# Kernel tuning notes

Measured on AMD Instinct MI355X. Metric: run time of the kernel, lower is better.

The kernel has to match this reference:

```python
import jax, jax.numpy as jnp
import numpy as np

B, L = 2, 2048
DIM, VOCAB, NL = 1024, 32000, 4
DSTATE, DCONV, EXPAND, HEADDIM = 128, 4, 2, 64
DIN = EXPAND * DIM            # 2048
H = DIN // HEADDIM            # 32 heads
CONVDIM = DIN + 2 * DSTATE    # 2304
DPROJ = 2 * DIN + 2 * DSTATE + H  # 4384
FFN = 4 * DIM                 # 4096
Q = 128                       # SSD chunk size
EPS = 1e-6


def _rms(x):
    return x * jax.lax.rsqrt(jnp.mean(x * x, axis=-1, keepdims=True) + EPS)


def _causal_conv(x, w, b):
    # x [B,L,C], depthwise causal conv, w [C,DCONV], b [C]
    y = jax.lax.conv_general_dilated(
        x.transpose(0, 2, 1), w[:, None, :], (1,), [(DCONV - 1, 0)],
        dimension_numbers=('NCH', 'OIH', 'NCH'), feature_group_count=CONVDIM)
    return (y + b[:, None]).transpose(0, 2, 1)


def _ssd(x, dt, A, Bm, Cm):
    # Exact selective scan h_t = h_{t-1}*exp(dt_t*A) + dt_t * x_t B_t ; y_t = C_t . h_t
    # computed in chunked (SSD) matmul form. x [b,l,h,p], dt [b,l,h], A [h], Bm/Cm [b,l,n]
    b, l, h, p = x.shape
    n = Bm.shape[-1]
    c = l // Q
    xr = x.reshape(b, c, Q, h, p)
    dtr = dt.reshape(b, c, Q, h)
    ar = (dt * A).reshape(b, c, Q, h)          # per-step log-decay (<= 0)
    Br = Bm.reshape(b, c, Q, n)
    Cr = Cm.reshape(b, c, Q, n)
    ca = jnp.cumsum(ar, axis=2)                # inclusive cumulative log-decay
    # ---- intra-chunk: causal decay-weighted 'attention' ----
    cah = ca.transpose(0, 1, 3, 2)             # [b,c,h,Q]
    idx = jnp.arange(Q)
    mask = idx[:, None] >= idx[None, :]
    diff = jnp.where(mask[None, None, None], cah[..., :, None] - cah[..., None, :], -jnp.inf)
    M = jnp.exp(diff)                          # [b,c,h,Q,Q]
    CB = jnp.einsum('bcin,bcjn->bcij', Cr, Br)
    T = CB[:, :, None] * M                     # [b,c,h,Q,Q]
    y_intra = jnp.einsum('bchij,bcjh,bcjhp->bcihp', T, dtr, xr)
    # ---- chunk-final states ----
    w = jnp.exp(ca[:, :, -1:, :] - ca) * dtr   # [b,c,Q,h]
    states = jnp.einsum('bcjh,bcjn,bcjhp->bchpn', w, Br, xr)
    chunk_decay = jnp.exp(ca[:, :, -1, :])     # [b,c,h]
    def step(s, inp):
        cd, st = inp
        prev = s
        s = s * cd[:, :, None, None] + st
        return s, prev
    s0 = jnp.zeros((b, h, p, n), x.dtype)
    _, s_prev = jax.lax.scan(step, s0, (chunk_decay.transpose(1, 0, 2),
                                        states.transpose(1, 0, 2, 3, 4)))
    s_prev = s_prev.transpose(1, 0, 2, 3, 4)   # [b,c,h,p,n] state entering each chunk
    y_inter = jnp.einsum('bcih,bcin,bchpn->bcihp', jnp.exp(ca), Cr, s_prev)
    return (y_intra + y_inter).reshape(b, l, h, p)


def _mamba(x, Wi, cw, cb, dtb, Alog, Dp, nw, Wo):
    bsz, sl, _ = x.shape
    zxbcdt = x @ Wi.T                          # [b,l,DPROJ]
    z = zxbcdt[..., :DIN]
    xBC = zxbcdt[..., DIN:DIN + CONVDIM]
    dtraw = zxbcdt[..., DIN + CONVDIM:]
    xBC = jax.nn.silu(_causal_conv(xBC, cw, cb))
    xs = xBC[..., :DIN]
    Bm = xBC[..., DIN:DIN + DSTATE]
    Cm = xBC[..., DIN + DSTATE:]
    dt = jax.nn.softplus(dtraw + dtb)
    A = -jnp.exp(Alog)
    x4 = xs.reshape(bsz, sl, H, HEADDIM)
    y = _ssd(x4, dt, A, Bm, Cm) + Dp[None, None, :, None] * x4
    y = y.reshape(bsz, sl, DIN)
    yg = y * jax.nn.silu(z)                    # gated RMSNorm (norm_before_gate=False)
    y = _rms(yg) * nw
    return y @ Wo.T


def _forward(tokens, embedding, lm_head_bias, in_proj_w, conv_w, conv_b,
             dt_bias, A_log, D, mnorm_w, out_proj_w, u_w, v_w, o_w):
    x = embedding[tokens]
    for li in range(NL):
        for _ in range(2):  # original applies each (mamba, ffn) pair twice
            x = _rms(x)
            x = x + _mamba(x, in_proj_w[li], conv_w[li], conv_b[li], dt_bias[li],
                           A_log[li], D[li], mnorm_w[li], out_proj_w[li])
            x = _rms(x)
            x = x + ((x @ u_w[li].T) * (x @ v_w[li].T)) @ o_w[li].T  # SGLU, dropout=0
    return x @ embedding.T + lm_head_bias      # tied lm_head


def setup_inputs():
    key = jax.random.key(0)
    ks = jax.random.split(key, 16)
    s = 0.02
    return {
        'tokens': jax.random.randint(ks[0], (B, L), 0, VOCAB),
        'embedding': jax.random.normal(ks[1], (VOCAB, DIM), jnp.float32) * s,
        'lm_head_bias': jnp.zeros((VOCAB,), jnp.float32),
        'in_proj_w': jax.random.normal(ks[2], (NL, DPROJ, DIM), jnp.float32) * s,
        'conv_w': jax.random.normal(ks[3], (NL, CONVDIM, DCONV), jnp.float32) * 0.2,
        'conv_b': jnp.zeros((NL, CONVDIM), jnp.float32),
        'dt_bias': jax.random.normal(ks[4], (NL, H), jnp.float32) * 0.3 - 3.0,
        'A_log': jnp.log(jax.random.uniform(ks[5], (NL, H), jnp.float32, 1.0, 16.0)),
        'D': jnp.ones((NL, H), jnp.float32) + 0.1 * jax.random.normal(ks[6], (NL, H), jnp.float32),
        'mnorm_w': jnp.ones((NL, DIN), jnp.float32),
        'out_proj_w': jax.random.normal(ks[7], (NL, DIM, DIN), jnp.float32) * s,
        'u_w': jax.random.normal(ks[8], (NL, FFN, DIM), jnp.float32) * s,
        'v_w': jax.random.normal(ks[9], (NL, FFN, DIM), jnp.float32) * s,
        'o_w': jax.random.normal(ks[10], (NL, DIM, FFN), jnp.float32) * s,
    }


def reference(tokens, embedding, lm_head_bias, in_proj_w, conv_w, conv_b,
              dt_bias, A_log, D, mnorm_w, out_proj_w, u_w, v_w, o_w):
    return _forward(tokens, embedding, lm_head_bias, in_proj_w, conv_w, conv_b,
                    dt_bias, A_log, D, mnorm_w, out_proj_w, u_w, v_w, o_w)
```

## Files before the change

### kernel.cpp

```cpp
#include <hip/hip_runtime.h>
#include <hip/hip_bf16.h>

#define BSZ 2
#define LSEQ 2048
#define DIM 1024
#define VOCAB 32000
#define NLAYER 4
#define DSTATE 128
#define DCONV 4
#define HEADDIM 64
#define DIN 2048
#define NH 32
#define CONVDIM 2304
#define DPROJ 4384
#define FFN 4096
#define QLEN 128
#define NTOK 4096
#define NCHUNK 32
#define CPB 16
#define DTOFF 4352

#define SMEM_BYTES 147456
#define SMEM2 131072

using f32x4 = __attribute__((ext_vector_type(4))) float;
using f16   = _Float16;
using f16x4 = __attribute__((ext_vector_type(4))) _Float16;
using f16x8 = __attribute__((ext_vector_type(8))) _Float16;

__device__ __forceinline__ void gld16(const void* g, void* l) {
  __builtin_amdgcn_global_load_lds(
      (const __attribute__((address_space(1))) unsigned int*)g,
      (__attribute__((address_space(3))) unsigned int*)l, 16, 0, 0);
}

__device__ __forceinline__ void swz_tiles(int& bx, int& by) {
  const int nx = gridDim.x, ny = gridDim.y;
  const int nwg = nx * ny;
  int bid = blockIdx.y * nx + blockIdx.x;
  if ((nwg & 7) == 0) bid = (bid & 7) * (nwg >> 3) + (bid >> 3);
  const int CW = 8;
  const int nchx = nx / CW;
  const int per = CW * ny;
  const int ch = bid / per;
  if (ch < nchx) {
    int wi = bid - ch * per;
    bx = ch * CW + (wi & (CW - 1));
    by = wi / CW;
  } else {
    int tb = bid - nchx * per;
    int tw = nx - nchx * CW;
    bx = nchx * CW + (tb % tw);
    by = tb / tw;
  }
}

template <int MODE>
__global__ __launch_bounds__(512, 2) void gemm_p(
    const f16* __restrict__ A, const f16* __restrict__ B,
    f16* __restrict__ Cg, float* __restrict__ Cf,
    float* __restrict__ dtr, const float* __restrict__ bias,
    int N, int Ksub, int lda, int ldb, int ldc)
{
  extern __shared__ char smem[];
  const int tid  = threadIdx.x;
  const int lane = tid & 63;
  const int wid  = tid >> 6;
  int bx, by; swz_tiles(bx, by);
  const int m0 = by * 256;
  const int n0 = bx * 128;
  const size_t kbase = (size_t)blockIdx.z * Ksub;
  if (gridDim.z > 1) Cg += (size_t)blockIdx.z * (size_t)gridDim.y * 256 * ldc;
  const int NT = Ksub >> 6;

  int arA[4], acA[4];
#pragma unroll
  for (int L = 0; L < 4; ++L) {
    int q = L * 512 + tid;
    int row = q >> 3;
    arA[L] = m0 + row;
    acA[L] = ((q & 7) ^ (row & 7)) << 3;
  }
  int brB[2], bcB[2];
#pragma unroll
  for (int L = 0; L < 2; ++L) {
    int q = L * 512 + tid;
    int row = q >> 3;
    int r = n0 + row; if (r > N - 1) r = N - 1;
    brB[L] = r;
    bcB[L] = ((q & 7) ^ (row & 7)) << 3;
  }

  auto stage = [&](int tt) {
    const int b = tt - (tt / 3) * 3;
    char* Ad = smem + b * 32768;
    char* Bd = smem + 98304 + b * 16384;
    const int kb = tt << 6;
#pragma unroll
    for (int L = 0; L < 4; ++L)
      gld16(A + (size_t)arA[L] * lda + kbase + kb + acA[L], Ad + (L * 512 + tid) * 16);
#pragma unroll
    for (int L = 0; L < 2; ++L)
      gld16(B + (size_t)brB[L] * ldb + kbase + kb + bcB[L], Bd + (L * 512 + tid) * 16);
  };

  const int wm = (wid >> 1) << 6;
  const int wn = (wid & 1) << 6;
  const int fr = lane & 15;
  const int kg = lane >> 4;

  f32x4 acc[4][4] = {};

  stage(0);
  stage(1);

  for (int t = 0; t < NT; ++t) {
    const int b = t - (t / 3) * 3;
    if (t + 1 < NT) {
      asm volatile("s_waitcnt vmcnt(6)" ::: "memory");
    } else {
      asm volatile("s_waitcnt vmcnt(0)" ::: "memory");
    }
    __builtin_amdgcn_s_barrier();
    asm volatile("" ::: "memory");
    if (t + 2 < NT) stage(t + 2);
    const f16* Ab = (const f16*)(smem + b * 32768);
    const f16* Bb = (const f16*)(smem + 98304 + b * 16384);
#pragma unroll
    for (int s = 0; s < 2; ++s) {
      f16x8 af[4], bf[4];
#pragma unroll
      for (int j = 0; j < 4; ++j) {
        int row = wm + j * 16 + fr;
        int g = kg + s * 4;
        af[j] = *(const f16x8*)&Ab[row * 64 + ((g ^ (row & 7)) << 3)];
      }
#pragma unroll
      for (int i = 0; i < 4; ++i) {
        int row = wn + i * 16 + fr;
        int g = kg + s * 4;
        bf[i] = *(const f16x8*)&Bb[row * 64 + ((g ^ (row & 7)) << 3)];
      }
      __builtin_amdgcn_s_setprio(1);
#pragma unroll
      for (int i = 0; i < 4; ++i)
#pragma unroll
        for (int j = 0; j < 4; ++j)
          acc[i][j] = __builtin_amdgcn_mfma_f32_16x16x32_f16(bf[i], af[j], acc[i][j], 0, 0, 0);
      __builtin_amdgcn_s_setprio(0);
    }
    asm volatile("" ::: "memory");
  }

  const int c4 = kg << 2;
#pragma unroll
  for (int i = 0; i < 4; ++i) {
    const int col = n0 + wn + i * 16 + c4;
    if (col >= N) continue;
#pragma unroll
    for (int j = 0; j < 4; ++j) {
      const int row = m0 + wm + j * 16 + fr;
      if constexpr (MODE == 1) {
        f32x4 bv = bias ? *(const f32x4*)(bias + col) : f32x4{0, 0, 0, 0};
        *(f32x4*)(Cf + (size_t)row * ldc + col) = acc[i][j] + bv;
      } else {
        f16x4 h;
#pragma unroll
        for (int r = 0; r < 4; ++r) h[r] = (f16)acc[i][j][r];
        *(f16x4*)(Cg + (size_t)row * ldc + col) = h;
        if (dtr && col >= DTOFF)
          *(f32x4*)(dtr + (size_t)row * NH + (col - DTOFF)) = acc[i][j];
      }
    }
  }
}

__global__ __launch_bounds__(512, 2) void gemm_uv2(
    const f16* __restrict__ A, const f16* __restrict__ Bu, const f16* __restrict__ Bv,
    f16* __restrict__ Gh)
{
  extern __shared__ char smem[];
  const int tid  = threadIdx.x;
  const int lane = tid & 63;
  const int wid  = tid >> 6;
  int bx, by; swz_tiles(bx, by);
  const int m0 = by * 256;
  const int n0 = bx * 128;
  const int NT = DIM >> 6;

  int arA[4], acA[4];
  const f16* bp[4];
  int bcB[4];
#pragma unroll
  for (int L = 0; L < 4; ++L) {
    int q = L * 512 + tid;
    int row = q >> 3;
    arA[L] = m0 + row;
    acA[L] = ((q & 7) ^ (row & 7)) << 3;
    bcB[L] = acA[L];
    bp[L] = (row < 128) ? (Bu + (size_t)(n0 + row) * DIM)
                        : (Bv + (size_t)(n0 + row - 128) * DIM);
  }

  auto stage = [&](int tt) {
    const int b = tt & 1;
    char* Ad = smem + b * 65536;
    char* Bd = Ad + 32768;
    const int kb = tt << 6;
#pragma unroll
    for (int L = 0; L < 4; ++L)
      gld16(A + (size_t)arA[L] * DIM + kb + acA[L], Ad + (L * 512 + tid) * 16);
#pragma unroll
    for (int L = 0; L < 4; ++L)
      gld16(bp[L] + kb + bcB[L], Bd + (L * 512 + tid) * 16);
  };

  const int wm = (wid >> 1) << 6;
  const int wn = (wid & 1) << 6;
  const int fr = lane & 15;
  const int kg = lane >> 4;

  f32x4 accu[4][4] = {}, accv[4][4] = {};

  stage(0);

  for (int t = 0; t < NT; ++t) {
    if (t + 1 < NT) {
      stage(t + 1);
      asm volatile("s_waitcnt vmcnt(8)" ::: "memory");
    } else {
      asm volatile("s_waitcnt vmcnt(0)" ::: "memory");
    }
    __builtin_amdgcn_s_barrier();
    asm volatile("" ::: "memory");
    const f16* Ab = (const f16*)(smem + (t & 1) * 65536);
    const f16* Bb = Ab + 16384;
#pragma unroll
    for (int s = 0; s < 2; ++s) {
      const int g = kg + s * 4;
      f16x8 af[4], bfu[4], bfv[4];
#pragma unroll
      for (int j = 0; j < 4; ++j) {
        int row = wm + j * 16 + fr;
        af[j] = *(const f16x8*)&Ab[row * 64 + ((g ^ (row & 7)) << 3)];
      }
#pragma unroll
      for (int i = 0; i < 4; ++i) {
        int ru = wn + i * 16 + fr;
        int rv = 128 + wn + i * 16 + fr;
        bfu[i] = *(const f16x8*)&Bb[ru * 64 + ((g ^ (ru & 7)) << 3)];
        bfv[i] = *(const f16x8*)&Bb[rv * 64 + ((g ^ (rv & 7)) << 3)];
      }
      __builtin_amdgcn_s_setprio(1);
#pragma unroll
      for (int i = 0; i < 4; ++i)
#pragma unroll
        for (int j = 0; j < 4; ++j) {
          accu[i][j] = __builtin_amdgcn_mfma_f32_16x16x32_f16(bfu[i], af[j], accu[i][j], 0, 0, 0);
          accv[i][j] = __builtin_amdgcn_mfma_f32_16x16x32_f16(bfv[i], af[j], accv[i][j], 0, 0, 0);
        }
      __builtin_amdgcn_s_setprio(0);
    }
    asm volatile("" ::: "memory");
    __builtin_amdgcn_s_barrier();
    asm volatile("" ::: "memory");
  }

  const int c4 = kg << 2;
#pragma unroll
  for (int i = 0; i < 4; ++i) {
    const int col = n0 + wn + i * 16 + c4;
#pragma unroll
    for (int j = 0; j < 4; ++j) {
      const int row = m0 + wm + j * 16 + fr;
      f16x4 h;
#pragma unroll
      for (int r = 0; r < 4; ++r)
        h[r] = (f16)(accu[i][j][r] * accv[i][j][r]);
      *(f16x4*)(Gh + (size_t)row * FFN + col) = h;
    }
  }
}

template <bool DORMS>
__global__ __launch_bounds__(256) void reduce_rms(const f16* __restrict__ parts,
                                                  const float* __restrict__ resid,
                                                  float* __restrict__ xn,
                                                  f16* __restrict__ outh, int np)
{
  const int row = blockIdx.x, tid = threadIdx.x;
  const size_t base = (size_t)row * DIM + tid * 4;
  f32x4 s = *(const f32x4*)(resid + base);
  for (int p = 0; p < np; ++p) {
    f16x4 pv = *(const f16x4*)(parts + (size_t)p * (NTOK * DIM) + base);
#pragma unroll
    for (int c = 0; c < 4; ++c) s[c] += (float)pv[c];
  }
  if constexpr (!DORMS) {
    f16x4 h;
#pragma unroll
    for (int c = 0; c < 4; ++c) h[c] = (f16)s[c];
    *(f16x4*)(outh + base) = h;
    return;
  }
  float ss = s[0] * s[0] + s[1] * s[1] + s[2] * s[2] + s[3] * s[3];
  for (int o = 32; o; o >>= 1) ss += __shfl_down(ss, o);
  __shared__ float red[4];
  if ((tid & 63) == 0) red[tid >> 6] = ss;
  __syncthreads();
  ss = red[0] + red[1] + red[2] + red[3];
  const float sc = rsqrtf(ss * (1.f / 1024.f) + 1e-6f);
  f32x4 o4 = s * sc;
  *(f32x4*)(xn + base) = o4;
  f16x4 h;
#pragma unroll
  for (int c = 0; c < 4; ++c) h[c] = (f16)o4[c];
  *(f16x4*)(outh + base) = h;
}

__global__ __launch_bounds__(256) void cvt_f2h_k(const float* __restrict__ src,
                                                 f16* __restrict__ dst, int n)
{
  for (size_t i = ((size_t)blockIdx.x * 256 + threadIdx.x) * 4; i < (size_t)n;
       i += (size_t)gridDim.x * 1024) {
    f32x4 v = *(const f32x4*)(src + i);
    f16x4 o;
#pragma unroll
    for (int c = 0; c < 4; ++c) o[c] = (f16)v[c];
    *(f16x4*)(dst + i) = o;
  }
}

__global__ __launch_bounds__(256) void cvt_wts(
    const float* __restrict__ inw, const float* __restrict__ outw,
    const float* __restrict__ uw, const float* __restrict__ vw,
    const float* __restrict__ ow,
    f16* __restrict__ w_in, f16* __restrict__ w_out,
    f16* __restrict__ w_uv, f16* __restrict__ w_o)
{
  const int b = blockIdx.x;
  const float* src; f16* dst;
  if (b < 17536) {
    int li = b / 4384, ib = b - li * 4384;
    src = inw  + (size_t)li * 4489216 + (size_t)ib * 1024;
    dst = w_in + (size_t)li * 4489216 + (size_t)ib * 1024;
  } else if (b < 25728) {
    int lb = b - 17536, li = lb >> 11, ib = lb & 2047;
    src = outw  + (size_t)li * 2097152 + (size_t)ib * 1024;
    dst = w_out + (size_t)li * 2097152 + (size_t)ib * 1024;
  } else if (b < 42112) {
    int lb = b - 25728, li = lb >> 12, ib = lb & 4095;
    src = uw   + (size_t)li * 4194304 + (size_t)ib * 1024;
    dst = w_uv + (size_t)li * 8388608 + (size_t)ib * 1024;
  } else if (b < 58496) {
    int lb = b - 42112, li = lb >> 12, ib = lb & 4095;
    src = vw   + (size_t)li * 4194304 + (size_t)ib * 1024;
    dst = w_uv + (size_t)li * 8388608 + 4194304 + (size_t)ib * 1024;
  } else {
    int lb = b - 58496, li = lb >> 12, ib = lb & 4095;
    src = ow  + (size_t)li * 4194304 + (size_t)ib * 1024;
    dst = w_o + (size_t)li * 4194304 + (size_t)ib * 1024;
  }
  const size_t i = (size_t)threadIdx.x * 4;
  f32x4 v = *(const f32x4*)(src + i);
  f16x4 o;
#pragma unroll
  for (int c = 0; c < 4; ++c) o[c] = (f16)v[c];
  *(f16x4*)(dst + i) = o;
}

__global__ __launch_bounds__(256) void gather_k(const int* __restrict__ tok,
                                                const float* __restrict__ emb,
                                                float* __restrict__ x)
{
  const int row = blockIdx.x;
  const int t = tok[row];
  const f32x4* s = (const f32x4*)(emb + (size_t)t * DIM);
  f32x4* d = (f32x4*)(x + (size_t)row * DIM);
  d[threadIdx.x] = s[threadIdx.x];
}

__global__ __launch_bounds__(256) void rms1024(const float* __restrict__ in,
                                               float* __restrict__ outf,
                                               f16* __restrict__ outh)
{
  const int row = blockIdx.x, tid = threadIdx.x;
  f32x4 v = ((const f32x4*)(in + (size_t)row * DIM))[tid];
  float ss = v[0] * v[0] + v[1] * v[1] + v[2] * v[2] + v[3] * v[3];
  for (int o = 32; o; o >>= 1) ss += __shfl_down(ss, o);
  __shared__ float red[4];
  if ((tid & 63) == 0) red[tid >> 6] = ss;
  __syncthreads();
  ss = red[0] + red[1] + red[2] + red[3];
  const float sc = rsqrtf(ss * (1.f / 1024.f) + 1e-6f);
  f32x4 o4 = v * sc;
  ((f32x4*)(outf + (size_t)row * DIM))[tid] = o4;
  f16x4 h;
#pragma unroll
  for (int c = 0; c < 4; ++c) h[c] = (f16)o4[c];
  ((f16x4*)(outh + (size_t)row * DIM))[tid] = h;
}

__global__ __launch_bounds__(256) void convdt(const f16* __restrict__ zx,
                                              const float* __restrict__ dtrw,
                                              const float* __restrict__ cw,
                                              const float* __restrict__ cbias,
                                              const float* __restrict__ dtb,
                                              const float* __restrict__ alog,
                                              f16* __restrict__ xbc,
                                              float* __restrict__ dt,
                                              float* __restrict__ ca)
{
  if (blockIdx.x < 576) {
    const int sid = blockIdx.x * 256 + threadIdx.x;
    const int c0 = (sid % 576) * 4;
    const int t0 = (sid / 576) * 16;
    float w[4][4], bs[4];
#pragma unroll
    for (int cc = 0; cc < 4; ++cc) {
      f32x4 wv = *(const f32x4*)(cw + (size_t)(c0 + cc) * 4);
      w[cc][0] = wv[0]; w[cc][1] = wv[1]; w[cc][2] = wv[2]; w[cc][3] = wv[3];
      bs[cc] = cbias[c0 + cc];
    }
    const int l0 = t0 & (LSEQ - 1);
    float x3[4] = {}, x2[4] = {}, x1[4] = {};
    if (l0 != 0) {
      f16x4 a = *(const f16x4*)(zx + (size_t)(t0 - 3) * DPROJ + DIN + c0);
      f16x4 b = *(const f16x4*)(zx + (size_t)(t0 - 2) * DPROJ + DIN + c0);
      f16x4 d = *(const f16x4*)(zx + (size_t)(t0 - 1) * DPROJ + DIN + c0);
#pragma unroll
      for (int c = 0; c < 4; ++c) { x3[c] = (float)a[c]; x2[c] = (float)b[c]; x1[c] = (float)d[c]; }
    }
    for (int i = 0; i < 16; ++i) {
      const int t = t0 + i;
      f16x4 xcv = *(const f16x4*)(zx + (size_t)t * DPROJ + DIN + c0);
      f16x4 o;
#pragma unroll
      for (int cc = 0; cc < 4; ++cc) {
        float xc = (float)xcv[cc];
        float a = bs[cc] + x3[cc] * w[cc][0] + x2[cc] * w[cc][1] +
                  x1[cc] * w[cc][2] + xc * w[cc][3];
        o[cc] = (f16)(a / (1.f + expf(-a)));
        x3[cc] = x2[cc]; x2[cc] = x1[cc]; x1[cc] = xc;
      }
      *(f16x4*)(xbc + (size_t)t * CONVDIM + c0) = o;
    }
  } else {
    const int loc = (threadIdx.x >> 7) * 128;
    const int u = (blockIdx.x - 576) * 2 + (threadIdx.x >> 7);
    const int bc = u >> 5, h = u & 31, q = threadIdx.x & 127;
    const int t = bc * 128 + q;
    float raw = dtrw[(size_t)t * NH + h] + dtb[h];
    float d = raw > 20.f ? raw : log1pf(expf(raw));
    dt[t * 32 + h] = d;
    float a = -expf(alog[h]) * d;
    __shared__ float s[256];
    s[loc + q] = a;
    __syncthreads();
    for (int off = 1; off < 128; off <<= 1) {
      float v = (q >= off) ? s[loc + q - off] : 0.f;
      __syncthreads();
      s[loc + q] += v;
      __syncthreads();
    }
    ca[(size_t)u * 128 + q] = s[loc + q];
  }
}

__global__ __launch_bounds__(256) void cb_mfma(const f16* __restrict__ xbc,
                                               float* __restrict__ CBo)
{
  const int bc = blockIdx.x;
  __shared__ f16 Cm[128 * 72], Bm[128 * 72];
  const int tid = threadIdx.x, lane = tid & 63, wid = tid >> 6;
  const int fr = lane & 15, kg = lane >> 4;
  f32x4 acc[2][8] = {};
  const int i = tid & 127;
  const f16* rowp = xbc + (size_t)(bc * 128 + i) * CONVDIM + DIN;

  for (int kh = 0; kh < 2; ++kh) {
#pragma unroll
    for (int it = 0; it < 8; ++it) {
      int idx = it * 256 + tid;
      int n0 = (idx >> 7) * 4;
      *(f16x4*)&Bm[i * 72 + n0] = *(const f16x4*)(rowp + kh * 64 + n0);
      *(f16x4*)&Cm[i * 72 + n0] = *(const f16x4*)(rowp + DSTATE + kh * 64 + n0);
    }
    __syncthreads();
#pragma unroll
    for (int kf = 0; kf < 2; ++kf) {
      const int ko = kf * 32 + kg * 8;
      f16x8 cf[2], bf[8];
#pragma unroll
      for (int ii = 0; ii < 2; ++ii)
        cf[ii] = *(const f16x8*)&Cm[((wid * 2 + ii) * 16 + fr) * 72 + ko];
#pragma unroll
      for (int jj = 0; jj < 8; ++jj)
        bf[jj] = *(const f16x8*)&Bm[(jj * 16 + fr) * 72 + ko];
      __builtin_amdgcn_s_setprio(1);
#pragma unroll
      for (int ii = 0; ii < 2; ++ii)
#pragma unroll
        for (int jj = 0; jj < 8; ++jj)
          acc[ii][jj] = __builtin_amdgcn_mfma_f32_16x16x32_f16(cf[ii], bf[jj], acc[ii][jj], 0, 0, 0);
      __builtin_amdgcn_s_setprio(0);
    }
    __syncthreads();
  }
  float* out = CBo + (size_t)bc * 16384;
#pragma unroll
  for (int ii = 0; ii < 2; ++ii) {
    const int i0 = (wid * 2 + ii) * 16 + kg * 4;
#pragma unroll
    for (int jj = 0; jj < 8; ++jj) {
      const int j = jj * 16 + fr;
#pragma unroll
      for (int r = 0; r < 4; ++r)
        out[(size_t)(i0 + r) * 128 + j] = acc[ii][jj][r];
    }
  }
}

__global__ __launch_bounds__(256) void ssd_states(const f16* __restrict__ xbc,
                                                  const float* __restrict__ dt,
                                                  const float* __restrict__ ca,
                                                  float* __restrict__ ST)
{
  const int bc = blockIdx.x >> 5, h = blockIdx.x & 31;
  __shared__ f16 Am[128 * 136];
  __shared__ f16 Bm[64 * 136];
  __shared__ float warr[128];
  const int tid = threadIdx.x, lane = tid & 63, wid = tid >> 6;
  if (tid < 128) {
    float cv = ca[(size_t)blockIdx.x * 128 + tid];
    float cl = ca[(size_t)blockIdx.x * 128 + 127];
    warr[tid] = expf(cl - cv) * dt[(size_t)(bc * 128 + tid) * 32 + h];
  }
  __syncthreads();
  {
    const int j = tid & 127;
    const float wj = warr[j];
    const f16* br = xbc + (size_t)(bc * 128 + j) * CONVDIM + DIN;
#pragma unroll
    for (int it = 0; it < 16; ++it) {
      int idx = it * 256 + tid;
      int n0 = (idx >> 7) * 4;
      f16x4 v = *(const f16x4*)(br + n0);
#pragma unroll
      for (int c = 0; c < 4; ++c) Am[(n0 + c) * 136 + j] = (f16)((float)v[c] * wj);
    }
    const f16* xr = xbc + (size_t)(bc * 128 + j) * CONVDIM + h * 64;
#pragma unroll
    for (int it = 0; it < 8; ++it) {
      int idx = it * 256 + tid;
      int p0 = (idx >> 7) * 4;
      f16x4 v = *(const f16x4*)(xr + p0);
#pragma unroll
      for (int c = 0; c < 4; ++c) Bm[(p0 + c) * 136 + j] = v[c];
    }
  }
  __syncthreads();
  const int fr = lane & 15, kg = lane >> 4;
  f32x4 acc[2][4] = {};
#pragma unroll
  for (int kf = 0; kf < 4; ++kf) {
    const int ko = kf * 32 + kg * 8;
    f16x8 bw[2], xf[4];
#pragma unroll
    for (int ii = 0; ii < 2; ++ii)
      bw[ii] = *(const f16x8*)&Am[((wid * 2 + ii) * 16 + fr) * 136 + ko];
#pragma unroll
    for (int pi = 0; pi < 4; ++pi)
      xf[pi] = *(const f16x8*)&Bm[(pi * 16 + fr) * 136 + ko];
    __builtin_amdgcn_s_setprio(1);
#pragma unroll
    for (int ii = 0; ii < 2; ++ii)
#pragma unroll
      for (int pi = 0; pi < 4; ++pi)
        acc[ii][pi] = __builtin_amdgcn_mfma_f32_16x16x32_f16(bw[ii], xf[pi], acc[ii][pi], 0, 0, 0);
    __builtin_amdgcn_s_setprio(0);
  }
  float* sb = ST + (size_t)blockIdx.x * 8192;
#pragma unroll
  for (int ii = 0; ii < 2; ++ii) {
    const int n0 = (wid * 2 + ii) * 16 + kg * 4;
#pragma unroll
    for (int pi = 0; pi < 4; ++pi) {
      const int p = pi * 16 + fr;
      *(f32x4*)(sb + (size_t)p * 128 + n0) = acc[ii][pi];
    }
  }
}

__global__ __launch_bounds__(256) void scan_k(const float* __restrict__ ca,
                                              float* __restrict__ states)
{
  const int b = blockIdx.x >> 10, h = (blockIdx.x >> 5) & 31, seg = blockIdx.x & 31;
  const int e = seg * 256 + threadIdx.x;
  float s = 0.f;
  for (int c = 0; c < CPB; ++c) {
    int bc = b * CPB + c;
    float cd = expf(ca[(size_t)(bc * 32 + h) * 128 + 127]);
    size_t idx = (size_t)(bc * 32 + h) * 8192 + e;
    float v = states[idx];
    states[idx] = s;
    s = s * cd + v;
  }
}

__global__ __launch_bounds__(256) void ssd_y(const f16* __restrict__ xbc,
                                             const float* __restrict__ dt,
                                             const float* __restrict__ ca,
                                             const float* __restrict__ CB,
                                             const float* __restrict__ Dvec,
                                             const float* __restrict__ ST,
                                             f16* __restrict__ ybuf)
{
  const int bc = blockIdx.x >> 5, h = blockIdx.x & 31;
  __shared__ f16 Am[128 * 136];
  __shared__ f16 Bm[64 * 136];
  __shared__ float cas[128], dtl[128];
  const int tid = threadIdx.x, lane = tid & 63, wid = tid >> 6;
  if (tid < 128) {
    cas[tid] = ca[(size_t)blockIdx.x * 128 + tid];
    dtl[tid] = dt[(size_t)(bc * 128 + tid) * 32 + h];
  }
  __syncthreads();
  {
    const int j = tid & 127;
    const float dj = dtl[j];
    const f16* xr = xbc + (size_t)(bc * 128 + j) * CONVDIM + h * 64;
#pragma unroll
    for (int it = 0; it < 8; ++it) {
      int idx = it * 256 + tid;
      int p0 = (idx >> 7) * 4;
      f16x4 v = *(const f16x4*)(xr + p0);
#pragma unroll
      for (int c = 0; c < 4; ++c) Bm[(p0 + c) * 136 + j] = (f16)((float)v[c] * dj);
    }
  }
  {
    const int i = tid >> 1;
    const int jh = (tid & 1) * 64;
    const float cai = cas[i];
    const float* cbr = CB + (size_t)bc * 16384 + (size_t)i * 128 + jh;
#pragma unroll
    for (int g = 0; g < 8; ++g) {
      int j0 = g * 8;
      f32x4 v0 = *(const f32x4*)(cbr + j0);
      f32x4 v1 = *(const f32x4*)(cbr + j0 + 4);
      f16x8 tv;
#pragma unroll
      for (int c = 0; c < 8; ++c) {
        int j = jh + j0 + c;
        float cbv = (c < 4) ? v0[c] : v1[c - 4];
        float val = (j <= i) ? cbv * expf(cai - cas[j]) : 0.f;
        tv[c] = (f16)val;
      }
      *(f16x8*)&Am[i * 136 + jh + j0] = tv;
    }
  }
  __syncthreads();
  const int fr = lane & 15, kg = lane >> 4;
  f32x4 a1[2][4] = {}, a2[2][4] = {};
#pragma unroll
  for (int kf = 0; kf < 4; ++kf) {
    const int ko = kf * 32 + kg * 8;
    f16x8 xf[4], tf[2];
#pragma unroll
    for (int pi = 0; pi < 4; ++pi)
      xf[pi] = *(const f16x8*)&Bm[(pi * 16 + fr) * 136 + ko];
#pragma unroll
    for (int ii = 0; ii < 2; ++ii)
      tf[ii] = *(const f16x8*)&Am[((wid * 2 + ii) * 16 + fr) * 136 + ko];
    __builtin_amdgcn_s_setprio(1);
#pragma unroll
    for (int ii = 0; ii < 2; ++ii)
#pragma unroll
      for (int pi = 0; pi < 4; ++pi)
        a1[ii][pi] = __builtin_amdgcn_mfma_f32_16x16x32_f16(xf[pi], tf[ii], a1[ii][pi], 0, 0, 0);
    __builtin_amdgcn_s_setprio(0);
  }
  __syncthreads();
  {
    const int i = tid & 127;
    const f16* cr = xbc + (size_t)(bc * 128 + i) * CONVDIM + DIN + DSTATE;
#pragma unroll
    for (int it = 0; it < 16; ++it) {
      int idx = it * 256 + tid;
      int n0 = (idx >> 7) * 4;
      *(f16x4*)&Am[i * 136 + n0] = *(const f16x4*)(cr + n0);
    }
    const float* sr = ST + (size_t)blockIdx.x * 8192;
    const int p = tid & 63;
#pragma unroll
    for (int it = 0; it < 8; ++it) {
      int idx = it * 256 + tid;
      int n0 = (idx >> 6) * 4;
      f32x4 v = *(const f32x4*)(sr + (size_t)p * 128 + n0);
      f16x4 hv;
#pragma unroll
      for (int c = 0; c < 4; ++c) hv[c] = (f16)v[c];
      *(f16x4*)&Bm[p * 136 + n0] = hv;
    }
  }
  __syncthreads();
#pragma unroll
  for (int kf = 0; kf < 4; ++kf) {
    const int ko = kf * 32 + kg * 8;
    f16x8 sf[4], cf[2];
#pragma unroll
    for (int pi = 0; pi < 4; ++pi)
      sf[pi] = *(const f16x8*)&Bm[(pi * 16 + fr) * 136 + ko];
#pragma unroll
    for (int ii = 0; ii < 2; ++ii)
      cf[ii] = *(const f16x8*)&Am[((wid * 2 + ii) * 16 + fr) * 136 + ko];
    __builtin_amdgcn_s_setprio(1);
#pragma unroll
    for (int ii = 0; ii < 2; ++ii)
#pragma unroll
      for (int pi = 0; pi < 4; ++pi)
        a2[ii][pi] = __builtin_amdgcn_mfma_f32_16x16x32_f16(sf[pi], cf[ii], a2[ii][pi], 0, 0, 0);
    __builtin_amdgcn_s_setprio(0);
  }
  const float dh = Dvec[h];
#pragma unroll
  for (int ii = 0; ii < 2; ++ii) {
    const int i = (wid * 2 + ii) * 16 + fr;
    const float ei = expf(cas[i]);
    const int tg = bc * 128 + i;
#pragma unroll
    for (int pi = 0; pi < 4; ++pi) {
      const int p0 = pi * 16 + kg * 4;
      f16x4 xv = *(const f16x4*)(xbc + (size_t)tg * CONVDIM + h * 64 + p0);
      f16x4 yo;
#pragma unroll
      for (int r = 0; r < 4; ++r)
        yo[r] = (f16)(a1[ii][pi][r] + ei * a2[ii][pi][r] + dh * (float)xv[r]);
      *(f16x4*)(ybuf + (size_t)tg * DIN + h * 64 + p0) = yo;
    }
  }
}

__global__ __launch_bounds__(256) void gate_rms(const f16* __restrict__ ybuf,
                                                const f16* __restrict__ zx,
                                                const float* __restrict__ nw,
                                                f16* __restrict__ outh)
{
  const int row = blockIdx.x, tid = threadIdx.x;
  f16x8 yv = *(const f16x8*)(ybuf + (size_t)row * DIN + tid * 8);
  f16x8 zv = *(const f16x8*)(zx + (size_t)row * DPROJ + tid * 8);
  float g[8];
  float ss = 0.f;
#pragma unroll
  for (int c = 0; c < 8; ++c) {
    float z = (float)zv[c];
    g[c] = (float)yv[c] * (z / (1.f + expf(-z)));
    ss += g[c] * g[c];
  }
  for (int o = 32; o; o >>= 1) ss += __shfl_down(ss, o);
  __shared__ float red[4];
  if ((tid & 63) == 0) red[tid >> 6] = ss;
  __syncthreads();
  ss = red[0] + red[1] + red[2] + red[3];
  const float sc = rsqrtf(ss * (1.f / 2048.f) + 1e-6f);
  f32x4 w0 = *(const f32x4*)(nw + tid * 8);
  f32x4 w1 = *(const f32x4*)(nw + tid * 8 + 4);
  f16x8 h;
#pragma unroll
  for (int c = 0; c < 8; ++c) {
    float w = (c < 4) ? w0[c] : w1[c - 4];
    h[c] = (f16)(g[c] * sc * w);
  }
  *(f16x8*)(outh + (size_t)row * DIN + tid * 8) = h;
}

extern "C" void kernel_launch(void* const* d_in, const int* in_sizes, int n_in,
                              void* d_out, int out_size, void* d_ws, size_t ws_size,
                              hipStream_t stream)
{
  (void)in_sizes; (void)n_in; (void)out_size; (void)ws_size;
  const int*   tokens = (const int*)d_in[0];
  const float* emb    = (const float*)d_in[1];
  const float* lmb    = (const float*)d_in[2];
  const float* inw    = (const float*)d_in[3];
  const float* cw     = (const float*)d_in[4];
  const float* cbias  = (const float*)d_in[5];
  const float* dtb    = (const float*)d_in[6];
  const float* alog   = (const float*)d_in[7];
  const float* Dvec   = (const float*)d_in[8];
  const float* nw     = (const float*)d_in[9];
  const float* outw   = (const float*)d_in[10];
  const float* uw     = (const float*)d_in[11];
  const float* vw     = (const float*)d_in[12];
  const float* ow     = (const float*)d_in[13];

  char* ws = (char*)d_ws;
  size_t off = 0;
  auto alloc = [&](size_t bytes) { void* p = ws + off; off += (bytes + 255) & ~(size_t)255; return p; };
  f16* emb_h   = (f16*)alloc((size_t)VOCAB * DIM * 2);
  float* xbuf  = (float*)alloc((size_t)NTOK * DIM * 4);
  float* xn    = (float*)alloc((size_t)NTOK * DIM * 4);
  f16* xnh     = (f16*)alloc((size_t)NTOK * DIM * 2);
  f16* xh_lm   = (f16*)alloc((size_t)NTOK * DIM * 2);
  float* dtraw = (float*)alloc((size_t)NTOK * NH * 4);
  float* dtbuf = (float*)alloc((size_t)NTOK * NH * 4);
  float* cabuf = (float*)alloc((size_t)NCHUNK * NH * QLEN * 4);
  float* CBbuf = (float*)alloc((size_t)NCHUNK * QLEN * QLEN * 4);
  f16* abh     = (f16*)alloc((size_t)NTOK * FFN * 2);

  char* ob = (char*)d_out;
  float* states = (float*)(ob);
  f16* zxb      = (f16*)(ob + 40000000);
  f16* xbc      = (f16*)(ob + 80000000);
  f16* ybuf     = (f16*)(ob + 100000000);
  f16* parts    = (f16*)(ob + 120000000);
  f16* w_in     = (f16*)(ob + 160000000);
  f16* w_out    = (f16*)(ob + 196000000);
  f16* w_uv     = (f16*)(ob + 213000000);
  f16* w_o      = (f16*)(ob + 281000000);

  cvt_f2h_k<<<4096, 256, 0, stream>>>(emb, emb_h, VOCAB * DIM);
  cvt_wts<<<74880, 256, 0, stream>>>(inw, outw, uw, vw, ow, w_in, w_out, w_uv, w_o);
  gather_k<<<NTOK, 256, 0, stream>>>(tokens, emb, xbuf);
  rms1024<<<NTOK, 256, 0, stream>>>(xbuf, xn, xnh);

  for (int it = 0; it < 2 * NLAYER; ++it) {
    const int li = it >> 1;
    const f16* w_inL  = w_in  + (size_t)li * 4489216;
    const f16* w_outL = w_out + (size_t)li * 2097152;
    const f16* w_uL   = w_uv  + (size_t)li * 8388608;
    const f16* w_vL   = w_uL  + 4194304;
    const f16* w_oL   = w_o   + (size_t)li * 4194304;
    gemm_p<0><<<dim3((DPROJ + 127) / 128, NTOK / 256, 1), 512, SMEM_BYTES, stream>>>(
        xnh, w_inL, zxb, nullptr, dtraw, nullptr, DPROJ, DIM, DIM, DIM, DPROJ);
    convdt<<<1088, 256, 0, stream>>>(zxb, dtraw, cw + (size_t)li * CONVDIM * DCONV,
                                     cbias + (size_t)li * CONVDIM,
                                     dtb + li * NH, alog + li * NH, xbc, dtbuf, cabuf);
    cb_mfma<<<NCHUNK, 256, 0, stream>>>(xbc, CBbuf);
    ssd_states<<<NCHUNK * NH, 256, 0, stream>>>(xbc, dtbuf, cabuf, states);
    scan_k<<<2048, 256, 0, stream>>>(cabuf, states);
    ssd_y<<<NCHUNK * NH, 256, 0, stream>>>(xbc, dtbuf, cabuf, CBbuf,
                                           Dvec + li * NH, states, ybuf);
    gate_rms<<<NTOK, 256, 0, stream>>>(ybuf, zxb, nw + (size_t)li * DIN, abh);
    gemm_p<0><<<dim3(DIM / 128, NTOK / 256, 2), 512, SMEM_BYTES, stream>>>(
        abh, w_outL, parts, nullptr, nullptr, nullptr, DIM, DIN / 2, DIN, DIN, DIM);
    reduce_rms<true><<<NTOK, 256, 0, stream>>>(parts, xn, xn, xnh, 2);
    gemm_uv2<<<dim3(FFN / 128, NTOK / 256, 1), 512, SMEM2, stream>>>(
        xnh, w_uL, w_vL, abh);
    gemm_p<0><<<dim3(DIM / 128, NTOK / 256, 2), 512, SMEM_BYTES, stream>>>(
        abh, w_oL, parts, nullptr, nullptr, nullptr, DIM, FFN / 2, FFN, FFN, DIM);
    if (it < 2 * NLAYER - 1)
      reduce_rms<true><<<NTOK, 256, 0, stream>>>(parts, xn, xn, xnh, 2);
    else
      reduce_rms<false><<<NTOK, 256, 0, stream>>>(parts, xn, nullptr, xh_lm, 2);
  }

  gemm_p<1><<<dim3(VOCAB / 128, NTOK / 256, 1), 512, SMEM_BYTES, stream>>>(
      xh_lm, emb_h, nullptr, (float*)d_out, nullptr, lmb, VOCAB, DIM, DIM, DIM, VOCAB);
}
```

Measured before the change: 3.084 ms.

## Use 256x256 GEMM tiles with K32 stages and 4-way split-K projections

```diff
diff --git a/kernel.cpp b/kernel.cpp
--- a/kernel.cpp
+++ b/kernel.cpp
@@ -20,7 +20,7 @@
 #define CPB 16
 #define DTOFF 4352
 
-#define SMEM_BYTES 147456
+#define SMEM3 98304
 #define SMEM2 131072
 
 using f32x4 = __attribute__((ext_vector_type(4))) float;
@@ -56,7 +56,7 @@
 }
 
 template <int MODE>
-__global__ __launch_bounds__(512, 2) void gemm_p(
+__global__ __launch_bounds__(512, 2) void gemm_p3(
     const f16* __restrict__ A, const f16* __restrict__ B,
     f16* __restrict__ Cg, float* __restrict__ Cf,
     float* __restrict__ dtr, const float* __restrict__ bias,
@@ -68,48 +68,42 @@
   const int wid  = tid >> 6;
   int bx, by; swz_tiles(bx, by);
   const int m0 = by * 256;
-  const int n0 = bx * 128;
+  const int n0 = bx * 256;
   const size_t kbase = (size_t)blockIdx.z * Ksub;
   if (gridDim.z > 1) Cg += (size_t)blockIdx.z * (size_t)gridDim.y * 256 * ldc;
-  const int NT = Ksub >> 6;
-
-  int arA[4], acA[4];
-#pragma unroll
-  for (int L = 0; L < 4; ++L) {
-    int q = L * 512 + tid;
-    int row = q >> 3;
-    arA[L] = m0 + row;
-    acA[L] = ((q & 7) ^ (row & 7)) << 3;
-  }
-  int brB[2], bcB[2];
+  const int NT = Ksub >> 5;
+
+  int arA[2], acA[2], brB[2], bcB[2];
 #pragma unroll
   for (int L = 0; L < 2; ++L) {
     int q = L * 512 + tid;
-    int row = q >> 3;
-    int r = n0 + row; if (r > N - 1) r = N - 1;
+    int rl = q >> 2;
+    arA[L] = m0 + rl;
+    acA[L] = ((q & 3) ^ ((rl >> 1) & 3)) << 3;
+    int r = n0 + rl; if (r > N - 1) r = N - 1;
     brB[L] = r;
-    bcB[L] = ((q & 7) ^ (row & 7)) << 3;
+    bcB[L] = acA[L];
   }
 
   auto stage = [&](int tt) {
     const int b = tt - (tt / 3) * 3;
-    char* Ad = smem + b * 32768;
-    char* Bd = smem + 98304 + b * 16384;
-    const int kb = tt << 6;
-#pragma unroll
-    for (int L = 0; L < 4; ++L)
+    char* Ad = smem + b * 16384;
+    char* Bd = smem + 49152 + b * 16384;
+    const int kb = tt << 5;
+#pragma unroll
+    for (int L = 0; L < 2; ++L)
       gld16(A + (size_t)arA[L] * lda + kbase + kb + acA[L], Ad + (L * 512 + tid) * 16);
 #pragma unroll
     for (int L = 0; L < 2; ++L)
       gld16(B + (size_t)brB[L] * ldb + kbase + kb + bcB[L], Bd + (L * 512 + tid) * 16);
   };
 
-  const int wm = (wid >> 1) << 6;
-  const int wn = (wid & 1) << 6;
+  const int wm = (wid >> 2) << 7;
+  const int wn = (wid & 3) << 6;
   const int fr = lane & 15;
   const int kg = lane >> 4;
 
-  f32x4 acc[4][4] = {};
+  f32x4 acc[4][8] = {};
 
   stage(0);
   stage(1);
@@ -117,38 +111,33 @@
   for (int t = 0; t < NT; ++t) {
     const int b = t - (t / 3) * 3;
     if (t + 1 < NT) {
-      asm volatile("s_waitcnt vmcnt(6)" ::: "memory");
+      asm volatile("s_waitcnt vmcnt(4)" ::: "memory");
     } else {
       asm volatile("s_waitcnt vmcnt(0)" ::: "memory");
     }
     __builtin_amdgcn_s_barrier();
     asm volatile("" ::: "memory");
     if (t + 2 < NT) stage(t + 2);
-    const f16* Ab = (const f16*)(smem + b * 32768);
-    const f16* Bb = (const f16*)(smem + 98304 + b * 16384);
-#pragma unroll
-    for (int s = 0; s < 2; ++s) {
-      f16x8 af[4], bf[4];
-#pragma unroll
-      for (int j = 0; j < 4; ++j) {
-        int row = wm + j * 16 + fr;
-        int g = kg + s * 4;
-        af[j] = *(const f16x8*)&Ab[row * 64 + ((g ^ (row & 7)) << 3)];
-      }
-#pragma unroll
-      for (int i = 0; i < 4; ++i) {
-        int row = wn + i * 16 + fr;
-        int g = kg + s * 4;
-        bf[i] = *(const f16x8*)&Bb[row * 64 + ((g ^ (row & 7)) << 3)];
-      }
-      __builtin_amdgcn_s_setprio(1);
-#pragma unroll
-      for (int i = 0; i < 4; ++i)
-#pragma unroll
-        for (int j = 0; j < 4; ++j)
-          acc[i][j] = __builtin_amdgcn_mfma_f32_16x16x32_f16(bf[i], af[j], acc[i][j], 0, 0, 0);
-      __builtin_amdgcn_s_setprio(0);
-    }
+    const f16* Ab = (const f16*)(smem + b * 16384);
+    const f16* Bb = (const f16*)(smem + 49152 + b * 16384);
+    f16x8 af[8], bf[4];
+#pragma unroll
+    for (int j = 0; j < 8; ++j) {
+      int rl = wm + j * 16 + fr;
+      af[j] = *(const f16x8*)&Ab[rl * 32 + ((kg ^ ((rl >> 1) & 3)) << 3)];
+    }
+#pragma unroll
+    for (int i = 0; i < 4; ++i) {
+      int rl = wn + i * 16 + fr;
+      bf[i] = *(const f16x8*)&Bb[rl * 32 + ((kg ^ ((rl >> 1) & 3)) << 3)];
+    }
+    __builtin_amdgcn_s_setprio(1);
+#pragma unroll
+    for (int i = 0; i < 4; ++i)
+#pragma unroll
+      for (int j = 0; j < 8; ++j)
+        acc[i][j] = __builtin_amdgcn_mfma_f32_16x16x32_f16(bf[i], af[j], acc[i][j], 0, 0, 0);
+    __builtin_amdgcn_s_setprio(0);
     asm volatile("" ::: "memory");
   }
 
@@ -158,7 +147,7 @@
     const int col = n0 + wn + i * 16 + c4;
     if (col >= N) continue;
 #pragma unroll
-    for (int j = 0; j < 4; ++j) {
+    for (int j = 0; j < 8; ++j) {
       const int row = m0 + wm + j * 16 + fr;
       if constexpr (MODE == 1) {
         f32x4 bv = bias ? *(const f32x4*)(bias + col) : f32x4{0, 0, 0, 0};
@@ -832,7 +821,7 @@
     const f16* w_uL   = w_uv  + (size_t)li * 8388608;
     const f16* w_vL   = w_uL  + 4194304;
     const f16* w_oL   = w_o   + (size_t)li * 4194304;
-    gemm_p<0><<<dim3((DPROJ + 127) / 128, NTOK / 256, 1), 512, SMEM_BYTES, stream>>>(
+    gemm_p3<0><<<dim3((DPROJ + 255) / 256, NTOK / 256, 1), 512, SMEM3, stream>>>(
         xnh, w_inL, zxb, nullptr, dtraw, nullptr, DPROJ, DIM, DIM, DIM, DPROJ);
     convdt<<<1088, 256, 0, stream>>>(zxb, dtraw, cw + (size_t)li * CONVDIM * DCONV,
                                      cbias + (size_t)li * CONVDIM,
@@ -843,19 +832,19 @@
     ssd_y<<<NCHUNK * NH, 256, 0, stream>>>(xbc, dtbuf, cabuf, CBbuf,
                                            Dvec + li * NH, states, ybuf);
     gate_rms<<<NTOK, 256, 0, stream>>>(ybuf, zxb, nw + (size_t)li * DIN, abh);
-    gemm_p<0><<<dim3(DIM / 128, NTOK / 256, 2), 512, SMEM_BYTES, stream>>>(
-        abh, w_outL, parts, nullptr, nullptr, nullptr, DIM, DIN / 2, DIN, DIN, DIM);
-    reduce_rms<true><<<NTOK, 256, 0, stream>>>(parts, xn, xn, xnh, 2);
+    gemm_p3<0><<<dim3(DIM / 256, NTOK / 256, 4), 512, SMEM3, stream>>>(
+        abh, w_outL, parts, nullptr, nullptr, nullptr, DIM, DIN / 4, DIN, DIN, DIM);
+    reduce_rms<true><<<NTOK, 256, 0, stream>>>(parts, xn, xn, xnh, 4);
     gemm_uv2<<<dim3(FFN / 128, NTOK / 256, 1), 512, SMEM2, stream>>>(
         xnh, w_uL, w_vL, abh);
-    gemm_p<0><<<dim3(DIM / 128, NTOK / 256, 2), 512, SMEM_BYTES, stream>>>(
-        abh, w_oL, parts, nullptr, nullptr, nullptr, DIM, FFN / 2, FFN, FFN, DIM);
+    gemm_p3<0><<<dim3(DIM / 256, NTOK / 256, 4), 512, SMEM3, stream>>>(
+        abh, w_oL, parts, nullptr, nullptr, nullptr, DIM, FFN / 4, FFN, FFN, DIM);
     if (it < 2 * NLAYER - 1)
-      reduce_rms<true><<<NTOK, 256, 0, stream>>>(parts, xn, xn, xnh, 2);
+      reduce_rms<true><<<NTOK, 256, 0, stream>>>(parts, xn, xn, xnh, 4);
     else
-      reduce_rms<false><<<NTOK, 256, 0, stream>>>(parts, xn, nullptr, xh_lm, 2);
-  }
-
-  gemm_p<1><<<dim3(VOCAB / 128, NTOK / 256, 1), 512, SMEM_BYTES, stream>>>(
+      reduce_rms<false><<<NTOK, 256, 0, stream>>>(parts, xn, nullptr, xh_lm, 4);
+  }
+
+  gemm_p3<1><<<dim3(VOCAB / 256, NTOK / 256, 1), 512, SMEM3, stream>>>(
       xh_lm, emb_h, nullptr, (float*)d_out, nullptr, lmb, VOCAB, DIM, DIM, DIM, VOCAB);
 }
```

Result: slower. 3.278 ms (+6.3%).
